# Performance work log

Hardware: AMD Instinct MI355X
Metric: run time of the kernel (lower is better)

## Reference

```python
import jax, jax.numpy as jnp
import numpy as np

DIM = 1024
NUM_HEADS = 16
HEAD_DIM = DIM // NUM_HEADS
SCALE = HEAD_DIM ** -0.5


def setup_inputs() -> dict:
    key0 = jax.random.key(0)
    ks = jax.random.split(key0, 8)
    B, L, S = 2, 1024, 2048
    inp = {
        "query": jax.random.normal(ks[0], (B, L, DIM), dtype=jnp.float32),
        "key": jax.random.normal(ks[1], (B, S, DIM), dtype=jnp.float32),
        "value": jax.random.normal(ks[2], (B, S, DIM), dtype=jnp.float32),
        # projection weights, stored as [in, out] so x @ W matches torch Linear
        "Wq": jax.random.normal(ks[3], (DIM, DIM), dtype=jnp.float32) * (DIM ** -0.5),
        "Wk": jax.random.normal(ks[4], (DIM, DIM), dtype=jnp.float32) * (DIM ** -0.5),
        "Wv": jax.random.normal(ks[5], (DIM, DIM), dtype=jnp.float32) * (DIM ** -0.5),
        "Wo": jax.random.normal(ks[6], (DIM, DIM), dtype=jnp.float32) * (DIM ** -0.5),
        "bo": jax.random.normal(ks[7], (DIM,), dtype=jnp.float32) * 0.02,
    }
    return inp


def reference(query, key, value, Wq, Wk, Wv, Wo, bo):
    B, L, C = query.shape
    S = key.shape[1]
    H, D = NUM_HEADS, HEAD_DIM
    # QKV projections (no bias), split heads: [B, H, L/S, D]
    q = (query @ Wq).reshape(B, L, H, D).transpose(0, 2, 1, 3)
    k = (key @ Wk).reshape(B, S, H, D).transpose(0, 2, 1, 3)
    v = (value @ Wv).reshape(B, S, H, D).transpose(0, 2, 1, 3)
    # scaled dot-product attention (qk_norm=False -> identity)
    attn = jnp.einsum("bhld,bhsd->bhls", q * SCALE, k)
    attn = jax.nn.softmax(attn, axis=-1)
    x = jnp.einsum("bhls,bhsd->bhld", attn, v)
    x = x.transpose(0, 2, 1, 3).reshape(B, L, C)
    # output projection (with bias)
    return x @ Wo + bo
```

## Files before the change

### kernel.cpp

```cpp
#include <hip/hip_runtime.h>

namespace {

typedef _Float16 f16;
typedef __attribute__((ext_vector_type(2))) _Float16 f16x2;
typedef __attribute__((ext_vector_type(4))) _Float16 f16x4;
typedef __attribute__((ext_vector_type(8))) _Float16 f16x8;
typedef __attribute__((ext_vector_type(4))) float f32x4;
typedef __attribute__((ext_vector_type(16))) float f32x16;

constexpr int kDim   = 1024;
constexpr int kHeads = 16;
constexpr int kHd    = 64;
constexpr int kB     = 2;
constexpr int kL     = 1024;
constexpr int kS     = 2048;

__device__ inline void gload16(const f16* g, f16* l) {
  __builtin_amdgcn_global_load_lds(
      (const __attribute__((address_space(1))) void*)(g),
      (__attribute__((address_space(3))) void*)(l), 16, 0, 0);
}

struct PrepArgs {
  const float* csrc[3];
  f16* cdst[3];
  int cn[3];
  const float* w[4];
  f16* wt[4];
};

__global__ __launch_bounds__(256) void prep(PrepArgs a) {
  __shared__ float T[32][33];
  const int y = blockIdx.y;
  if (y < 3) {
    const int i = (blockIdx.x * 256 + threadIdx.x) * 8;
    if (i >= a.cn[y]) return;
    const float* __restrict__ src = a.csrc[y];
    float4 v0 = *(const float4*)(src + i);
    float4 v1 = *(const float4*)(src + i + 4);
    f16x8 h = {(f16)v0.x, (f16)v0.y, (f16)v0.z, (f16)v0.w,
               (f16)v1.x, (f16)v1.y, (f16)v1.z, (f16)v1.w};
    *(f16x8*)(a.cdst[y] + i) = h;
  } else {
    if (blockIdx.x >= 1024) return;
    const int z = y - 3;
    const float* __restrict__ W = a.w[z];
    f16* __restrict__ Wt = a.wt[z];
    const int n0 = (blockIdx.x & 31) * 32;
    const int k0 = (blockIdx.x >> 5) * 32;
    const int r = threadIdx.x >> 3;
    const int c = (threadIdx.x & 7) * 4;
    float4 v = *(const float4*)(W + (size_t)(k0 + r) * kDim + n0 + c);
    T[c + 0][r] = v.x; T[c + 1][r] = v.y; T[c + 2][r] = v.z; T[c + 3][r] = v.w;
    __syncthreads();
    f16x4 h = {(f16)T[r][c], (f16)T[r][c + 1], (f16)T[r][c + 2], (f16)T[r][c + 3]};
    *(f16x4*)(Wt + (size_t)(n0 + r) * kDim + k0 + c) = h;
  }
}

struct ProjArgs {
  const f16* A[3];
  const f16* Bt[3];
  f16* C[3];
};

__global__ __launch_bounds__(256) void gemm_proj(ProjArgs p) {
  constexpr int K = kDim;
  constexpr int NI = K / 32;
  int bx = (blockIdx.x & 7) * 80 + (blockIdx.x >> 3);
  int z, m0, n0, Nz;
  if (bx < 128)      { z = 0; m0 = (bx >> 3) * 128; n0 = (bx & 7) * 128; Nz = kDim; }
  else if (bx < 384) { bx -= 128; z = 1; m0 = (bx >> 3) * 128; n0 = (bx & 7) * 128; Nz = kDim; }
  else               { bx -= 384; z = 2; m0 = (bx >> 5) * 128; n0 = (bx & 31) * 128; Nz = kB * kS; }
  const f16* __restrict__ A  = p.A[z];
  const f16* __restrict__ Bt = p.Bt[z];
  f16* __restrict__ C = p.C[z];

  __shared__ __align__(16) f16 As[2][128 * 32];
  __shared__ __align__(16) f16 Bs[2][128 * 32];
  const int t = threadIdx.x;
  const int lane = t & 63;
  const int wave = t >> 6;
  const int wm = (wave >> 1) * 64;
  const int wn = (wave & 1) * 64;
  const int col = lane & 15;
  const int quad = lane >> 4;

  f32x4 acc[4][4];
#pragma unroll
  for (int i = 0; i < 4; ++i)
#pragma unroll
    for (int j = 0; j < 4; ++j) acc[i][j] = (f32x4){0.f, 0.f, 0.f, 0.f};

  const int c0 = t, c1 = t + 256;
  const f16* a0 = A + (size_t)(m0 + (c0 >> 2)) * K + (c0 & 3) * 8;
  const f16* a1 = A + (size_t)(m0 + (c1 >> 2)) * K + (c1 & 3) * 8;
  const f16* b0 = Bt + (size_t)(n0 + (c0 >> 2)) * K + (c0 & 3) * 8;
  const f16* b1 = Bt + (size_t)(n0 + (c1 >> 2)) * K + (c1 & 3) * 8;
  f16* const as0 = As[0] + c0 * 8;
  f16* const as1 = As[0] + c1 * 8;
  f16* const bs0 = Bs[0] + c0 * 8;
  f16* const bs1 = Bs[0] + c1 * 8;
  constexpr int kBuf = 128 * 32;

  gload16(a0, as0);
  gload16(a1, as1);
  gload16(b0, bs0);
  gload16(b1, bs1);
  __syncthreads();

  for (int i = 0; i < NI; ++i) {
    const int cur = i & 1;
    if (i + 1 < NI) {
      const int ko = (i + 1) * 32;
      const int nb = (1 - cur) * kBuf;
      gload16(a0 + ko, as0 + nb);
      gload16(a1 + ko, as1 + nb);
      gload16(b0 + ko, bs0 + nb);
      gload16(b1 + ko, bs1 + nb);
    }

    f16x8 af[4], bf[4];
#pragma unroll
    for (int mt = 0; mt < 4; ++mt)
      af[mt] = *(const f16x8*)(As[cur] + (wm + mt * 16 + col) * 32 + quad * 8);
#pragma unroll
    for (int nt = 0; nt < 4; ++nt)
      bf[nt] = *(const f16x8*)(Bs[cur] + (wn + nt * 16 + col) * 32 + quad * 8);
#pragma unroll
    for (int mt = 0; mt < 4; ++mt)
#pragma unroll
      for (int nt = 0; nt < 4; ++nt)
        acc[mt][nt] = __builtin_amdgcn_mfma_f32_16x16x32_f16(
            af[mt], bf[nt], acc[mt][nt], 0, 0, 0);

    __syncthreads();
  }

  const int crow = m0 + wm + quad * 4;
  const int ccol = n0 + wn + col;
#pragma unroll
  for (int mt = 0; mt < 4; ++mt)
#pragma unroll
    for (int nt = 0; nt < 4; ++nt)
#pragma unroll
      for (int r = 0; r < 4; ++r)
        C[(size_t)(crow + mt * 16 + r) * Nz + ccol + nt * 16] =
            (f16)acc[mt][nt][r];
}

__global__ __launch_bounds__(256) void gemm_out(
    const f16* __restrict__ A, const f16* __restrict__ Bt,
    const float* __restrict__ bias, float* __restrict__ C, int M, int N, int K)
{
  __shared__ __align__(16) f16 As[2][64 * 32];
  __shared__ __align__(16) f16 Bs[2][64 * 32];
  const int t = threadIdx.x;
  const int lane = t & 63;
  const int wave = t >> 6;
  const int swz = (blockIdx.x & 7) * 64 + (blockIdx.x >> 3);
  const int n0 = (swz & 15) * 64;
  const int m0 = (swz >> 4) * 64;
  const int wm = (wave >> 1) * 32;
  const int wn = (wave & 1) * 32;
  const int col = lane & 15;
  const int quad = lane >> 4;
  const int NI = K / 32;
  constexpr int kBuf = 64 * 32;

  f32x4 acc[2][2];
#pragma unroll
  for (int i = 0; i < 2; ++i)
#pragma unroll
    for (int j = 0; j < 2; ++j) acc[i][j] = (f32x4){0.f, 0.f, 0.f, 0.f};

  const f16* a0 = A + (size_t)(m0 + (t >> 2)) * K + (t & 3) * 8;
  const f16* b0 = Bt + (size_t)(n0 + (t >> 2)) * K + (t & 3) * 8;
  f16* const as0 = As[0] + t * 8;
  f16* const bs0 = Bs[0] + t * 8;

  gload16(a0, as0);
  gload16(b0, bs0);
  __syncthreads();

  for (int i = 0; i < NI; ++i) {
    const int cur = i & 1;
    if (i + 1 < NI) {
      const int ko = (i + 1) * 32;
      const int nb = (1 - cur) * kBuf;
      gload16(a0 + ko, as0 + nb);
      gload16(b0 + ko, bs0 + nb);
    }

    f16x8 af[2], bf[2];
#pragma unroll
    for (int mt = 0; mt < 2; ++mt)
      af[mt] = *(const f16x8*)(As[cur] + (wm + mt * 16 + col) * 32 + quad * 8);
#pragma unroll
    for (int nt = 0; nt < 2; ++nt)
      bf[nt] = *(const f16x8*)(Bs[cur] + (wn + nt * 16 + col) * 32 + quad * 8);
#pragma unroll
    for (int mt = 0; mt < 2; ++mt)
#pragma unroll
      for (int nt = 0; nt < 2; ++nt)
        acc[mt][nt] = __builtin_amdgcn_mfma_f32_16x16x32_f16(
            af[mt], bf[nt], acc[mt][nt], 0, 0, 0);

    __syncthreads();
  }

  const int crow = m0 + wm + quad * 4;
  const int ccol = n0 + wn + col;
#pragma unroll
  for (int mt = 0; mt < 2; ++mt)
#pragma unroll
    for (int nt = 0; nt < 2; ++nt) {
      const float bv = bias[ccol + nt * 16];
#pragma unroll
      for (int r = 0; r < 4; ++r)
        C[(size_t)(crow + mt * 16 + r) * N + ccol + nt * 16] =
            acc[mt][nt][r] + bv;
    }
}


__device__ inline unsigned pk2f(float a, float b) {
  union { f16x2 h; unsigned u; } c;
  c.h = f16x2{(f16)a, (f16)b};
  return c.u;
}

__device__ inline void swap32(unsigned& x, unsigned& y) {
  asm("v_permlane32_swap_b32 %0, %1" : "+v"(x), "+v"(y));
}

__global__ __launch_bounds__(256, 2) void flash_attn_mfma4(
    const f16* __restrict__ q, const f16* __restrict__ k,
    const f16* __restrict__ vT, f16* __restrict__ x)
{
  constexpr int LP  = 72;
  constexpr int NT2 = (kS / 2) / 64;
  __shared__ __align__(16) f16 Kt[2][2][64 * LP];
  __shared__ __align__(16) f16 Vt[2][2][64 * LP];

  const int t    = threadIdx.x;
  const int lane = t & 63;
  const int wave = t >> 6;
  const int wq   = wave & 1;
  const int wh   = wave >> 1;
  const int ln   = lane & 31;
  const int hi   = lane >> 5;
  const int bh   = blockIdx.x;
  const int l0   = blockIdx.y * 64;
  const int h    = bh & (kHeads - 1);
  const int b    = bh >> 4;

  f16x8 qf[4];
  {
    const f16* src = q + ((size_t)b * kL + l0 + wq * 32 + ln) * kDim + h * kHd + hi * 8;
#pragma unroll
    for (int ks = 0; ks < 4; ++ks) {
      qf[ks] = *(const f16x8*)(src + ks * 16);
#pragma unroll
      for (int u = 0; u < 8; ++u) qf[ks][u] *= (f16)0.125f;
    }
  }

  const int srow = t >> 2;
  const int scol = (t & 3) * 16;
  const f16* kb = k + ((size_t)b * kS + srow) * kDim + h * kHd + scol;
  const f16* vb = vT + ((size_t)(h * kHd + srow)) * (kB * kS) + b * kS + scol;
  const size_t kHalf = (size_t)1024 * kDim;

  f32x16 accO[2];
#pragma unroll
  for (int dt = 0; dt < 2; ++dt)
#pragma unroll
    for (int r = 0; r < 16; ++r) accO[dt][r] = 0.f;
  float lsum = 0.f;

  f16x8 kh0a, kh0b, kh1a, kh1b, vh0a, vh0b, vh1a, vh1b;

#define STAGE_LOAD(i)                                                   \
  { const f16* kp0 = kb + (size_t)(i) * 64 * kDim;                      \
    const f16* kp1 = kp0 + kHalf;                                       \
    const f16* vp0 = vb + (i) * 64;                                     \
    const f16* vp1 = vp0 + 1024;                                        \
    kh0a = *(const f16x8*)(kp0); kh0b = *(const f16x8*)(kp0 + 8);       \
    kh1a = *(const f16x8*)(kp1); kh1b = *(const f16x8*)(kp1 + 8);       \
    vh0a = *(const f16x8*)(vp0); vh0b = *(const f16x8*)(vp0 + 8);       \
    vh1a = *(const f16x8*)(vp1); vh1b = *(const f16x8*)(vp1 + 8); }

#define STAGE_WRITE(bf)                                                 \
  { f16* kd0 = &Kt[bf][0][srow * LP + scol];                            \
    f16* kd1 = &Kt[bf][1][srow * LP + scol];                            \
    f16* vd0 = &Vt[bf][0][srow * LP + scol];                            \
    f16* vd1 = &Vt[bf][1][srow * LP + scol];                            \
    *(f16x8*)(kd0) = kh0a; *(f16x8*)(kd0 + 8) = kh0b;                   \
    *(f16x8*)(kd1) = kh1a; *(f16x8*)(kd1 + 8) = kh1b;                   \
    *(f16x8*)(vd0) = vh0a; *(f16x8*)(vd0 + 8) = vh0b;                   \
    *(f16x8*)(vd1) = vh1a; *(f16x8*)(vd1 + 8) = vh1b; }

  STAGE_LOAD(0);
  STAGE_WRITE(0);

  for (int i = 0; i < NT2; ++i) {
    const int cur = i & 1;
    if (i + 1 < NT2) STAGE_LOAD(i + 1);
    __syncthreads();

    const f16* Kc = &Kt[cur][wh][0];
    const f16* Vc = &Vt[cur][wh][0];

    f16x8 pf[4];
#pragma unroll
    for (int sub = 0; sub < 2; ++sub) {
      f32x16 s;
#pragma unroll
      for (int r = 0; r < 16; ++r) s[r] = 0.f;
      __builtin_amdgcn_s_setprio(1);
#pragma unroll
      for (int ks = 0; ks < 4; ++ks) {
        f16x8 kf = *(const f16x8*)(Kc + (sub * 32 + ln) * LP + ks * 16 + hi * 8);
        s = __builtin_amdgcn_mfma_f32_32x32x16_f16(kf, qf[ks], s, 0, 0, 0);
      }
      __builtin_amdgcn_s_setprio(0);

      float pp[16];
#pragma unroll
      for (int r = 0; r < 16; ++r) { pp[r] = __expf(s[r]); lsum += pp[r]; }

#pragma unroll
      for (int kk = 0; kk < 2; ++kk) {
        unsigned a0 = pk2f(pp[8 * kk + 0], pp[8 * kk + 1]);
        unsigned a1 = pk2f(pp[8 * kk + 2], pp[8 * kk + 3]);
        unsigned b0 = pk2f(pp[8 * kk + 4], pp[8 * kk + 5]);
        unsigned b1 = pk2f(pp[8 * kk + 6], pp[8 * kk + 7]);
        swap32(a0, b0);
        swap32(a1, b1);
        union { unsigned u[4]; f16x8 v; } w;
        w.u[0] = a0; w.u[1] = a1; w.u[2] = b0; w.u[3] = b1;
        pf[sub * 2 + kk] = w.v;
      }
    }

    __builtin_amdgcn_s_setprio(1);
#pragma unroll
    for (int dt = 0; dt < 2; ++dt)
#pragma unroll
      for (int ks = 0; ks < 4; ++ks) {
        f16x8 vf = *(const f16x8*)(Vc + (dt * 32 + ln) * LP + ks * 16 + hi * 8);
        accO[dt] = __builtin_amdgcn_mfma_f32_32x32x16_f16(pf[ks], vf, accO[dt], 0, 0, 0);
      }
    __builtin_amdgcn_s_setprio(0);

    if (i + 1 < NT2) STAGE_WRITE(1 - cur);
  }
#undef STAGE_LOAD
#undef STAGE_WRITE

  lsum += __shfl_xor(lsum, 32);
  __syncthreads();
  float* sc = (float*)&Kt[0][0][0];
  float* sl = sc + 128 * 33;
  if (wh == 1) {
    float* dst = sc + (wq * 64 + lane) * 33;
#pragma unroll
    for (int dt = 0; dt < 2; ++dt)
#pragma unroll
      for (int r = 0; r < 16; ++r) dst[dt * 16 + r] = accO[dt][r];
    sl[wq * 64 + lane] = lsum;
  }
  __syncthreads();
  if (wh == 0) {
    const float* src = sc + (wq * 64 + lane) * 33;
#pragma unroll
    for (int dt = 0; dt < 2; ++dt)
#pragma unroll
      for (int r = 0; r < 16; ++r) accO[dt][r] += src[dt * 16 + r];
    const float inv = 1.f / (lsum + sl[wq * 64 + lane]);
    const size_t row0 = (size_t)b * kL + l0 + wq * 32;
    f16* xb = x + row0 * kDim + h * kHd + ln;
#pragma unroll
    for (int r = 0; r < 16; ++r) {
      const int qr = (r & 3) + 8 * (r >> 2) + 4 * hi;
      const float invr = __shfl(inv, qr);
      xb[(size_t)qr * kDim]      = (f16)(accO[0][r] * invr);
      xb[(size_t)qr * kDim + 32] = (f16)(accO[1][r] * invr);
    }
  }
}

}

extern "C" void kernel_launch(void* const* d_in, const int* in_sizes, int n_in,
                              void* d_out, int out_size, void* d_ws, size_t ws_size,
                              hipStream_t stream) {
  const float* query = (const float*)d_in[0];
  const float* key   = (const float*)d_in[1];
  const float* value = (const float*)d_in[2];
  const float* Wq    = (const float*)d_in[3];
  const float* Wk    = (const float*)d_in[4];
  const float* Wv    = (const float*)d_in[5];
  const float* Wo    = (const float*)d_in[6];
  const float* bo    = (const float*)d_in[7];
  float* out = (float*)d_out;

  f16* ws = (f16*)d_ws;
  f16* qh  = ws;
  f16* kh  = qh + (size_t)kB * kL * kDim;
  f16* vh  = kh + (size_t)kB * kS * kDim;
  f16* wqt = vh + (size_t)kB * kS * kDim;
  f16* wkt = wqt + (size_t)kDim * kDim;
  f16* wvt = wkt + (size_t)kDim * kDim;
  f16* wot = wvt + (size_t)kDim * kDim;
  f16* qp  = wot + (size_t)kDim * kDim;
  f16* kp  = qp + (size_t)kB * kL * kDim;
  f16* vpT = kp + (size_t)kB * kS * kDim;
  f16* xh  = vpT + (size_t)kB * kS * kDim;

  PrepArgs pr;
  pr.csrc[0] = query; pr.cdst[0] = qh; pr.cn[0] = kB * kL * kDim;
  pr.csrc[1] = key;   pr.cdst[1] = kh; pr.cn[1] = kB * kS * kDim;
  pr.csrc[2] = value; pr.cdst[2] = vh; pr.cn[2] = kB * kS * kDim;
  pr.w[0] = Wq; pr.wt[0] = wqt;
  pr.w[1] = Wk; pr.wt[1] = wkt;
  pr.w[2] = Wv; pr.wt[2] = wvt;
  pr.w[3] = Wo; pr.wt[3] = wot;
  prep<<<dim3(2048, 7), 256, 0, stream>>>(pr);

  ProjArgs pa;
  pa.A[0] = qh;  pa.Bt[0] = wqt; pa.C[0] = qp;
  pa.A[1] = kh;  pa.Bt[1] = wkt; pa.C[1] = kp;
  pa.A[2] = wvt; pa.Bt[2] = vh;  pa.C[2] = vpT;
  gemm_proj<<<dim3(640), 256, 0, stream>>>(pa);

  flash_attn_mfma4<<<dim3(kB * kHeads, kL / 64), 256, 0, stream>>>(
      qp, kp, vpT, xh);

  gemm_out<<<dim3(512), 256, 0, stream>>>(
      xh, wot, bo, out, kB * kL, kDim, kDim);
}
```

Measured before the change: 180.6 us.

## Triple-buffer projection GEMM LDS tiles with explicit vmcnt waits

The QKV projection GEMM moves from a double-buffered to a triple-buffered LDS pipeline. Two K-tiles are prefetched ahead, and each stage waits with a manual s_waitcnt vmcnt(4) plus a raw s_barrier instead of __syncthreads, so one prefetch can stay in flight while compute proceeds. This is meant to hide global load latency better, at the cost of 50% more shared memory (48KB), which may reduce occupancy. An unused variable declaration was also added in the attention loop.

```diff
diff --git a/kernel.cpp b/kernel.cpp
--- a/kernel.cpp
+++ b/kernel.cpp
@@ -77,8 +77,8 @@
   const f16* __restrict__ Bt = p.Bt[z];
   f16* __restrict__ C = p.C[z];
 
-  __shared__ __align__(16) f16 As[2][128 * 32];
-  __shared__ __align__(16) f16 Bs[2][128 * 32];
+  __shared__ __align__(16) f16 As[3][128 * 32];
+  __shared__ __align__(16) f16 Bs[3][128 * 32];
   const int t = threadIdx.x;
   const int lane = t & 63;
   const int wave = t >> 6;
@@ -104,39 +104,56 @@
   f16* const bs1 = Bs[0] + c1 * 8;
   constexpr int kBuf = 128 * 32;
 
-  gload16(a0, as0);
-  gload16(a1, as1);
-  gload16(b0, bs0);
-  gload16(b1, bs1);
-  __syncthreads();
-
-  for (int i = 0; i < NI; ++i) {
-    const int cur = i & 1;
-    if (i + 1 < NI) {
-      const int ko = (i + 1) * 32;
-      const int nb = (1 - cur) * kBuf;
-      gload16(a0 + ko, as0 + nb);
-      gload16(a1 + ko, as1 + nb);
-      gload16(b0 + ko, bs0 + nb);
-      gload16(b1 + ko, bs1 + nb);
-    }
-
-    f16x8 af[4], bf[4];
-#pragma unroll
-    for (int mt = 0; mt < 4; ++mt)
-      af[mt] = *(const f16x8*)(As[cur] + (wm + mt * 16 + col) * 32 + quad * 8);
-#pragma unroll
-    for (int nt = 0; nt < 4; ++nt)
-      bf[nt] = *(const f16x8*)(Bs[cur] + (wn + nt * 16 + col) * 32 + quad * 8);
-#pragma unroll
-    for (int mt = 0; mt < 4; ++mt)
-#pragma unroll
-      for (int nt = 0; nt < 4; ++nt)
-        acc[mt][nt] = __builtin_amdgcn_mfma_f32_16x16x32_f16(
-            af[mt], bf[nt], acc[mt][nt], 0, 0, 0);
-
-    __syncthreads();
-  }
+#define PSTAGE(nb, tile)                                            \
+  { const int ko = (tile) * 32;                                     \
+    gload16(a0 + ko, as0 + (nb) * kBuf);                            \
+    gload16(a1 + ko, as1 + (nb) * kBuf);                            \
+    gload16(b0 + ko, bs0 + (nb) * kBuf);                            \
+    gload16(b1 + ko, bs1 + (nb) * kBuf); }
+
+#define PCOMP(cur)                                                  \
+  { f16x8 af[4], bf[4];                                             \
+    _Pragma("unroll")                                               \
+    for (int mt = 0; mt < 4; ++mt)                                  \
+      af[mt] = *(const f16x8*)(As[cur] + (wm + mt * 16 + col) * 32 + quad * 8); \
+    _Pragma("unroll")                                               \
+    for (int nt = 0; nt < 4; ++nt)                                  \
+      bf[nt] = *(const f16x8*)(Bs[cur] + (wn + nt * 16 + col) * 32 + quad * 8); \
+    _Pragma("unroll")                                               \
+    for (int mt = 0; mt < 4; ++mt)                                  \
+      _Pragma("unroll")                                             \
+      for (int nt = 0; nt < 4; ++nt)                                \
+        acc[mt][nt] = __builtin_amdgcn_mfma_f32_16x16x32_f16(       \
+            af[mt], bf[nt], acc[mt][nt], 0, 0, 0); }
+
+#define PWAITBAR(N)                                                 \
+  __builtin_amdgcn_sched_barrier(0);                                \
+  asm volatile("s_waitcnt vmcnt(" #N ")" ::: "memory");             \
+  __builtin_amdgcn_s_barrier();                                     \
+  __builtin_amdgcn_sched_barrier(0);
+
+#define PITER(cur, nb, i)                                           \
+  PSTAGE(nb, (i) + 2);                                              \
+  PCOMP(cur);                                                       \
+  PWAITBAR(4)
+
+  PSTAGE(0, 0);
+  PSTAGE(1, 1);
+  PWAITBAR(4);
+
+  for (int ii = 0; ii < 10; ++ii) {
+    PITER(0, 2, ii * 3 + 0);
+    PITER(1, 0, ii * 3 + 1);
+    PITER(2, 1, ii * 3 + 2);
+  }
+  PCOMP(0);
+  PWAITBAR(0);
+  PCOMP(1);
+
+#undef PSTAGE
+#undef PCOMP
+#undef PWAITBAR
+#undef PITER
 
   const int crow = m0 + wm + quad * 4;
   const int ccol = n0 + wn + col;
@@ -307,6 +324,7 @@
 
   for (int i = 0; i < NT2; ++i) {
     const int cur = i & 1;
+    f16x8 nk0, nk1, nv0, nv1;
     if (i + 1 < NT2) STAGE_LOAD(i + 1);
     __syncthreads();
 
```

After: 191.6 us. 6.1% more time.

## Fuse fp32-to-fp16 activation conversion into projection GEMM loads

Applied to the files above, without the earlier changes.

Stops converting query/key/value to fp16 in the prep kernel. The projection GEMM now reads the fp32 activations directly, converts them in registers and writes them to LDS, while the fp16 weights keep using direct global-to-LDS loads. This removes a full write and re-read of the fp16 activation copies. In exchange, the fp32 tiles are loaded twice as many bytes per GEMM tile, they go through registers with extra convert and LDS store work in the main loop, and register pressure rises.

```diff
diff --git a/kernel.cpp b/kernel.cpp
--- a/kernel.cpp
+++ b/kernel.cpp
@@ -23,45 +23,29 @@
 }
 
 struct PrepArgs {
-  const float* csrc[3];
-  f16* cdst[3];
-  int cn[3];
   const float* w[4];
   f16* wt[4];
 };
 
 __global__ __launch_bounds__(256) void prep(PrepArgs a) {
   __shared__ float T[32][33];
-  const int y = blockIdx.y;
-  if (y < 3) {
-    const int i = (blockIdx.x * 256 + threadIdx.x) * 8;
-    if (i >= a.cn[y]) return;
-    const float* __restrict__ src = a.csrc[y];
-    float4 v0 = *(const float4*)(src + i);
-    float4 v1 = *(const float4*)(src + i + 4);
-    f16x8 h = {(f16)v0.x, (f16)v0.y, (f16)v0.z, (f16)v0.w,
-               (f16)v1.x, (f16)v1.y, (f16)v1.z, (f16)v1.w};
-    *(f16x8*)(a.cdst[y] + i) = h;
-  } else {
-    if (blockIdx.x >= 1024) return;
-    const int z = y - 3;
-    const float* __restrict__ W = a.w[z];
-    f16* __restrict__ Wt = a.wt[z];
-    const int n0 = (blockIdx.x & 31) * 32;
-    const int k0 = (blockIdx.x >> 5) * 32;
-    const int r = threadIdx.x >> 3;
-    const int c = (threadIdx.x & 7) * 4;
-    float4 v = *(const float4*)(W + (size_t)(k0 + r) * kDim + n0 + c);
-    T[c + 0][r] = v.x; T[c + 1][r] = v.y; T[c + 2][r] = v.z; T[c + 3][r] = v.w;
-    __syncthreads();
-    f16x4 h = {(f16)T[r][c], (f16)T[r][c + 1], (f16)T[r][c + 2], (f16)T[r][c + 3]};
-    *(f16x4*)(Wt + (size_t)(n0 + r) * kDim + k0 + c) = h;
-  }
+  const int z = blockIdx.y;
+  const float* __restrict__ W = a.w[z];
+  f16* __restrict__ Wt = a.wt[z];
+  const int n0 = (blockIdx.x & 31) * 32;
+  const int k0 = (blockIdx.x >> 5) * 32;
+  const int r = threadIdx.x >> 3;
+  const int c = (threadIdx.x & 7) * 4;
+  float4 v = *(const float4*)(W + (size_t)(k0 + r) * kDim + n0 + c);
+  T[c + 0][r] = v.x; T[c + 1][r] = v.y; T[c + 2][r] = v.z; T[c + 3][r] = v.w;
+  __syncthreads();
+  f16x4 h = {(f16)T[r][c], (f16)T[r][c + 1], (f16)T[r][c + 2], (f16)T[r][c + 3]};
+  *(f16x4*)(Wt + (size_t)(n0 + r) * kDim + k0 + c) = h;
 }
 
 struct ProjArgs {
-  const f16* A[3];
-  const f16* Bt[3];
+  const float* F[3];
+  const f16*   H[3];
   f16* C[3];
 };
 
@@ -73,12 +57,18 @@
   if (bx < 128)      { z = 0; m0 = (bx >> 3) * 128; n0 = (bx & 7) * 128; Nz = kDim; }
   else if (bx < 384) { bx -= 128; z = 1; m0 = (bx >> 3) * 128; n0 = (bx & 7) * 128; Nz = kDim; }
   else               { bx -= 384; z = 2; m0 = (bx >> 5) * 128; n0 = (bx & 31) * 128; Nz = kB * kS; }
-  const f16* __restrict__ A  = p.A[z];
-  const f16* __restrict__ Bt = p.Bt[z];
+  const float* __restrict__ F = p.F[z];
+  const f16*   __restrict__ H = p.H[z];
   f16* __restrict__ C = p.C[z];
+  const int frow0 = (z == 2) ? n0 : m0;
+  const int hrow0 = (z == 2) ? m0 : n0;
 
   __shared__ __align__(16) f16 As[2][128 * 32];
   __shared__ __align__(16) f16 Bs[2][128 * 32];
+  f16* const fls = (z == 2) ? &Bs[0][0] : &As[0][0];
+  f16* const hls = (z == 2) ? &As[0][0] : &Bs[0][0];
+  constexpr int kBuf = 128 * 32;
+
   const int t = threadIdx.x;
   const int lane = t & 63;
   const int wave = t >> 6;
@@ -94,40 +84,53 @@
     for (int j = 0; j < 4; ++j) acc[i][j] = (f32x4){0.f, 0.f, 0.f, 0.f};
 
   const int c0 = t, c1 = t + 256;
-  const f16* a0 = A + (size_t)(m0 + (c0 >> 2)) * K + (c0 & 3) * 8;
-  const f16* a1 = A + (size_t)(m0 + (c1 >> 2)) * K + (c1 & 3) * 8;
-  const f16* b0 = Bt + (size_t)(n0 + (c0 >> 2)) * K + (c0 & 3) * 8;
-  const f16* b1 = Bt + (size_t)(n0 + (c1 >> 2)) * K + (c1 & 3) * 8;
-  f16* const as0 = As[0] + c0 * 8;
-  f16* const as1 = As[0] + c1 * 8;
-  f16* const bs0 = Bs[0] + c0 * 8;
-  f16* const bs1 = Bs[0] + c1 * 8;
-  constexpr int kBuf = 128 * 32;
-
-  gload16(a0, as0);
-  gload16(a1, as1);
-  gload16(b0, bs0);
-  gload16(b1, bs1);
+  const float* Fg0 = F + (size_t)(frow0 + (c0 >> 2)) * K + (c0 & 3) * 8;
+  const float* Fg1 = F + (size_t)(frow0 + (c1 >> 2)) * K + (c1 & 3) * 8;
+  const f16*   Hg0 = H + (size_t)(hrow0 + (c0 >> 2)) * K + (c0 & 3) * 8;
+  const f16*   Hg1 = H + (size_t)(hrow0 + (c1 >> 2)) * K + (c1 & 3) * 8;
+  f16* const fd0 = fls + c0 * 8;
+  f16* const fd1 = fls + c1 * 8;
+  f16* const hd0 = hls + c0 * 8;
+  f16* const hd1 = hls + c1 * 8;
+
+  float4 fa0, fb0, fa1, fb1;
+
+#define FLOAD(i)                                                        \
+  { const float* f0 = Fg0 + (i) * 32; const float* f1 = Fg1 + (i) * 32; \
+    fa0 = *(const float4*)(f0); fb0 = *(const float4*)(f0 + 4);         \
+    fa1 = *(const float4*)(f1); fb1 = *(const float4*)(f1 + 4); }
+
+#define FWRITE(nb)                                                      \
+  { f16x8 h0 = {(f16)fa0.x, (f16)fa0.y, (f16)fa0.z, (f16)fa0.w,         \
+                (f16)fb0.x, (f16)fb0.y, (f16)fb0.z, (f16)fb0.w};        \
+    f16x8 h1 = {(f16)fa1.x, (f16)fa1.y, (f16)fa1.z, (f16)fa1.w,         \
+                (f16)fb1.x, (f16)fb1.y, (f16)fb1.z, (f16)fb1.w};        \
+    *(f16x8*)(fd0 + (nb) * kBuf) = h0;                                  \
+    *(f16x8*)(fd1 + (nb) * kBuf) = h1; }
+
+  FLOAD(0);
+  gload16(Hg0, hd0);
+  gload16(Hg1, hd1);
+  FWRITE(0);
   __syncthreads();
 
   for (int i = 0; i < NI; ++i) {
     const int cur = i & 1;
+    const int nxt = 1 - cur;
     if (i + 1 < NI) {
       const int ko = (i + 1) * 32;
-      const int nb = (1 - cur) * kBuf;
-      gload16(a0 + ko, as0 + nb);
-      gload16(a1 + ko, as1 + nb);
-      gload16(b0 + ko, bs0 + nb);
-      gload16(b1 + ko, bs1 + nb);
+      FLOAD(i + 1);
+      gload16(Hg0 + ko, hd0 + nxt * kBuf);
+      gload16(Hg1 + ko, hd1 + nxt * kBuf);
     }
 
     f16x8 af[4], bf[4];
 #pragma unroll
     for (int mt = 0; mt < 4; ++mt)
-      af[mt] = *(const f16x8*)(As[cur] + (wm + mt * 16 + col) * 32 + quad * 8);
+      af[mt] = *(const f16x8*)(&As[0][0] + cur * kBuf + (wm + mt * 16 + col) * 32 + quad * 8);
 #pragma unroll
     for (int nt = 0; nt < 4; ++nt)
-      bf[nt] = *(const f16x8*)(Bs[cur] + (wn + nt * 16 + col) * 32 + quad * 8);
+      bf[nt] = *(const f16x8*)(&Bs[0][0] + cur * kBuf + (wn + nt * 16 + col) * 32 + quad * 8);
 #pragma unroll
     for (int mt = 0; mt < 4; ++mt)
 #pragma unroll
@@ -135,8 +138,12 @@
         acc[mt][nt] = __builtin_amdgcn_mfma_f32_16x16x32_f16(
             af[mt], bf[nt], acc[mt][nt], 0, 0, 0);
 
+    if (i + 1 < NI) FWRITE(nxt);
     __syncthreads();
   }
+
+#undef FLOAD
+#undef FWRITE
 
   const int crow = m0 + wm + quad * 4;
   const int ccol = n0 + wn + col;
@@ -408,10 +415,7 @@
   float* out = (float*)d_out;
 
   f16* ws = (f16*)d_ws;
-  f16* qh  = ws;
-  f16* kh  = qh + (size_t)kB * kL * kDim;
-  f16* vh  = kh + (size_t)kB * kS * kDim;
-  f16* wqt = vh + (size_t)kB * kS * kDim;
+  f16* wqt = ws;
   f16* wkt = wqt + (size_t)kDim * kDim;
   f16* wvt = wkt + (size_t)kDim * kDim;
   f16* wot = wvt + (size_t)kDim * kDim;
@@ -421,19 +425,16 @@
   f16* xh  = vpT + (size_t)kB * kS * kDim;
 
   PrepArgs pr;
-  pr.csrc[0] = query; pr.cdst[0] = qh; pr.cn[0] = kB * kL * kDim;
-  pr.csrc[1] = key;   pr.cdst[1] = kh; pr.cn[1] = kB * kS * kDim;
-  pr.csrc[2] = value; pr.cdst[2] = vh; pr.cn[2] = kB * kS * kDim;
   pr.w[0] = Wq; pr.wt[0] = wqt;
   pr.w[1] = Wk; pr.wt[1] = wkt;
   pr.w[2] = Wv; pr.wt[2] = wvt;
   pr.w[3] = Wo; pr.wt[3] = wot;
-  prep<<<dim3(2048, 7), 256, 0, stream>>>(pr);
+  prep<<<dim3(1024, 4), 256, 0, stream>>>(pr);
 
   ProjArgs pa;
-  pa.A[0] = qh;  pa.Bt[0] = wqt; pa.C[0] = qp;
-  pa.A[1] = kh;  pa.Bt[1] = wkt; pa.C[1] = kp;
-  pa.A[2] = wvt; pa.Bt[2] = vh;  pa.C[2] = vpT;
+  pa.F[0] = query; pa.H[0] = wqt; pa.C[0] = qp;
+  pa.F[1] = key;   pa.H[1] = wkt; pa.C[1] = kp;
+  pa.F[2] = value; pa.H[2] = wvt; pa.C[2] = vpT;
   gemm_proj<<<dim3(640), 256, 0, stream>>>(pa);
 
   flash_attn_mfma4<<<dim3(kB * kHeads, kL / 64), 256, 0, stream>>>(
```

After: 192.0 us. 6.3% more time.

## Load K/V fragments straight from global in attention, drop LDS staging

Applied to the files above, without the earlier changes.

The attention kernel stops staging K and V tiles through double-buffered shared memory. Each wave now reads its MFMA fragments directly from global memory into registers, relying on L2 reuse and removing the per-tile barrier. The attention grid gets a swizzled 1D block order, and the output GEMM replaces direct-to-LDS loads with register-staged double buffering and drops its swizzle. Each wave now issues its own uncoalesced global loads with no explicit software prefetch, which risks exposed load latency and higher register pressure.

```diff
diff --git a/kernel.cpp b/kernel.cpp
--- a/kernel.cpp
+++ b/kernel.cpp
@@ -159,15 +159,13 @@
   const int t = threadIdx.x;
   const int lane = t & 63;
   const int wave = t >> 6;
-  const int swz = (blockIdx.x & 7) * 64 + (blockIdx.x >> 3);
-  const int n0 = (swz & 15) * 64;
-  const int m0 = (swz >> 4) * 64;
+  const int n0 = blockIdx.x * 64;
+  const int m0 = blockIdx.y * 64;
   const int wm = (wave >> 1) * 32;
   const int wn = (wave & 1) * 32;
   const int col = lane & 15;
   const int quad = lane >> 4;
   const int NI = K / 32;
-  constexpr int kBuf = 64 * 32;
 
   f32x4 acc[2][2];
 #pragma unroll
@@ -177,21 +175,23 @@
 
   const f16* a0 = A + (size_t)(m0 + (t >> 2)) * K + (t & 3) * 8;
   const f16* b0 = Bt + (size_t)(n0 + (t >> 2)) * K + (t & 3) * 8;
-  f16* const as0 = As[0] + t * 8;
-  f16* const bs0 = Bs[0] + t * 8;
-
-  gload16(a0, as0);
-  gload16(b0, bs0);
-  __syncthreads();
+
+  {
+    f16x8 ra0 = *(const f16x8*)(a0);
+    f16x8 rb0 = *(const f16x8*)(b0);
+    *(f16x8*)(As[0] + t * 8) = ra0;
+    *(f16x8*)(Bs[0] + t * 8) = rb0;
+  }
 
   for (int i = 0; i < NI; ++i) {
     const int cur = i & 1;
+    f16x8 na0, nb0;
     if (i + 1 < NI) {
       const int ko = (i + 1) * 32;
-      const int nb = (1 - cur) * kBuf;
-      gload16(a0 + ko, as0 + nb);
-      gload16(b0 + ko, bs0 + nb);
-    }
+      na0 = *(const f16x8*)(a0 + ko);
+      nb0 = *(const f16x8*)(b0 + ko);
+    }
+    __syncthreads();
 
     f16x8 af[2], bf[2];
 #pragma unroll
@@ -207,7 +207,11 @@
         acc[mt][nt] = __builtin_amdgcn_mfma_f32_16x16x32_f16(
             af[mt], bf[nt], acc[mt][nt], 0, 0, 0);
 
-    __syncthreads();
+    if (i + 1 < NI) {
+      const int nxt = 1 - cur;
+      *(f16x8*)(As[nxt] + t * 8) = na0;
+      *(f16x8*)(Bs[nxt] + t * 8) = nb0;
+    }
   }
 
   const int crow = m0 + wm + quad * 4;
@@ -235,14 +239,14 @@
   asm("v_permlane32_swap_b32 %0, %1" : "+v"(x), "+v"(y));
 }
 
-__global__ __launch_bounds__(256, 2) void flash_attn_mfma4(
+__global__ __launch_bounds__(256, 2) void flash_attn_mfma5(
     const f16* __restrict__ q, const f16* __restrict__ k,
     const f16* __restrict__ vT, f16* __restrict__ x)
 {
-  constexpr int LP  = 72;
   constexpr int NT2 = (kS / 2) / 64;
-  __shared__ __align__(16) f16 Kt[2][2][64 * LP];
-  __shared__ __align__(16) f16 Vt[2][2][64 * LP];
+  constexpr size_t kVRow = (size_t)kB * kS;
+  __shared__ float sc[128 * 33];
+  __shared__ float sl[128];
 
   const int t    = threadIdx.x;
   const int lane = t & 63;
@@ -251,8 +255,9 @@
   const int wh   = wave >> 1;
   const int ln   = lane & 31;
   const int hi   = lane >> 5;
-  const int bh   = blockIdx.x;
-  const int l0   = blockIdx.y * 64;
+  const int swz  = (blockIdx.x & 7) * 64 + (blockIdx.x >> 3);
+  const int bh   = swz >> 4;
+  const int l0   = (swz & 15) * 64;
   const int h    = bh & (kHeads - 1);
   const int b    = bh >> 4;
 
@@ -267,11 +272,8 @@
     }
   }
 
-  const int srow = t >> 2;
-  const int scol = (t & 3) * 16;
-  const f16* kb = k + ((size_t)b * kS + srow) * kDim + h * kHd + scol;
-  const f16* vb = vT + ((size_t)(h * kHd + srow)) * (kB * kS) + b * kS + scol;
-  const size_t kHalf = (size_t)1024 * kDim;
+  const f16* kb = k + ((size_t)b * kS + wh * 1024 + ln) * kDim + h * kHd + hi * 8;
+  const f16* vb = vT + ((size_t)(h * kHd + ln)) * kVRow + b * kS + wh * 1024 + hi * 8;
 
   f32x16 accO[2];
 #pragma unroll
@@ -280,38 +282,21 @@
     for (int r = 0; r < 16; ++r) accO[dt][r] = 0.f;
   float lsum = 0.f;
 
-  f16x8 kh0a, kh0b, kh1a, kh1b, vh0a, vh0b, vh1a, vh1b;
-
-#define STAGE_LOAD(i)                                                   \
-  { const f16* kp0 = kb + (size_t)(i) * 64 * kDim;                      \
-    const f16* kp1 = kp0 + kHalf;                                       \
-    const f16* vp0 = vb + (i) * 64;                                     \
-    const f16* vp1 = vp0 + 1024;                                        \
-    kh0a = *(const f16x8*)(kp0); kh0b = *(const f16x8*)(kp0 + 8);       \
-    kh1a = *(const f16x8*)(kp1); kh1b = *(const f16x8*)(kp1 + 8);       \
-    vh0a = *(const f16x8*)(vp0); vh0b = *(const f16x8*)(vp0 + 8);       \
-    vh1a = *(const f16x8*)(vp1); vh1b = *(const f16x8*)(vp1 + 8); }
-
-#define STAGE_WRITE(bf)                                                 \
-  { f16* kd0 = &Kt[bf][0][srow * LP + scol];                            \
-    f16* kd1 = &Kt[bf][1][srow * LP + scol];                            \
-    f16* vd0 = &Vt[bf][0][srow * LP + scol];                            \
-    f16* vd1 = &Vt[bf][1][srow * LP + scol];                            \
-    *(f16x8*)(kd0) = kh0a; *(f16x8*)(kd0 + 8) = kh0b;                   \
-    *(f16x8*)(kd1) = kh1a; *(f16x8*)(kd1 + 8) = kh1b;                   \
-    *(f16x8*)(vd0) = vh0a; *(f16x8*)(vd0 + 8) = vh0b;                   \
-    *(f16x8*)(vd1) = vh1a; *(f16x8*)(vd1 + 8) = vh1b; }
-
-  STAGE_LOAD(0);
-  STAGE_WRITE(0);
-
   for (int i = 0; i < NT2; ++i) {
-    const int cur = i & 1;
-    if (i + 1 < NT2) STAGE_LOAD(i + 1);
-    __syncthreads();
-
-    const f16* Kc = &Kt[cur][wh][0];
-    const f16* Vc = &Vt[cur][wh][0];
+    const f16* kp = kb + (size_t)i * 64 * kDim;
+    const f16* vp = vb + i * 64;
+
+    f16x8 kf[2][4], vf[2][4];
+#pragma unroll
+    for (int sub = 0; sub < 2; ++sub)
+#pragma unroll
+      for (int ks = 0; ks < 4; ++ks)
+        kf[sub][ks] = *(const f16x8*)(kp + (size_t)sub * 32 * kDim + ks * 16);
+#pragma unroll
+    for (int dt = 0; dt < 2; ++dt)
+#pragma unroll
+      for (int ks = 0; ks < 4; ++ks)
+        vf[dt][ks] = *(const f16x8*)(vp + (size_t)dt * 32 * kVRow + ks * 16);
 
     f16x8 pf[4];
 #pragma unroll
@@ -321,10 +306,8 @@
       for (int r = 0; r < 16; ++r) s[r] = 0.f;
       __builtin_amdgcn_s_setprio(1);
 #pragma unroll
-      for (int ks = 0; ks < 4; ++ks) {
-        f16x8 kf = *(const f16x8*)(Kc + (sub * 32 + ln) * LP + ks * 16 + hi * 8);
-        s = __builtin_amdgcn_mfma_f32_32x32x16_f16(kf, qf[ks], s, 0, 0, 0);
-      }
+      for (int ks = 0; ks < 4; ++ks)
+        s = __builtin_amdgcn_mfma_f32_32x32x16_f16(kf[sub][ks], qf[ks], s, 0, 0, 0);
       __builtin_amdgcn_s_setprio(0);
 
       float pp[16];
@@ -349,21 +332,12 @@
 #pragma unroll
     for (int dt = 0; dt < 2; ++dt)
 #pragma unroll
-      for (int ks = 0; ks < 4; ++ks) {
-        f16x8 vf = *(const f16x8*)(Vc + (dt * 32 + ln) * LP + ks * 16 + hi * 8);
-        accO[dt] = __builtin_amdgcn_mfma_f32_32x32x16_f16(pf[ks], vf, accO[dt], 0, 0, 0);
-      }
+      for (int ks = 0; ks < 4; ++ks)
+        accO[dt] = __builtin_amdgcn_mfma_f32_32x32x16_f16(pf[ks], vf[dt][ks], accO[dt], 0, 0, 0);
     __builtin_amdgcn_s_setprio(0);
-
-    if (i + 1 < NT2) STAGE_WRITE(1 - cur);
-  }
-#undef STAGE_LOAD
-#undef STAGE_WRITE
+  }
 
   lsum += __shfl_xor(lsum, 32);
-  __syncthreads();
-  float* sc = (float*)&Kt[0][0][0];
-  float* sl = sc + 128 * 33;
   if (wh == 1) {
     float* dst = sc + (wq * 64 + lane) * 33;
 #pragma unroll
@@ -436,9 +410,8 @@
   pa.A[2] = wvt; pa.Bt[2] = vh;  pa.C[2] = vpT;
   gemm_proj<<<dim3(640), 256, 0, stream>>>(pa);
 
-  flash_attn_mfma4<<<dim3(kB * kHeads, kL / 64), 256, 0, stream>>>(
-      qp, kp, vpT, xh);
-
-  gemm_out<<<dim3(512), 256, 0, stream>>>(
+  flash_attn_mfma5<<<dim3(512), 256, 0, stream>>>(qp, kp, vpT, xh);
+
+  gemm_out<<<dim3(kDim / 64, (kB * kL) / 64), 256, 0, stream>>>(
       xh, wot, bo, out, kB * kL, kDim, kDim);
 }
```

Measured after the change: 214.0 us. 1.18x slower.
